# Kernel optimization log

Hardware: AMD Instinct MI355X
Metric: run time of the kernel (lower is better)

Reference implementation:

```python
import jax, jax.numpy as jnp
import numpy as np

N, D, O, E = 8192, 1024, 1024, 16

def setup_inputs() -> dict:
    key = jax.random.key(0)
    k1, k2, k3, k4 = jax.random.split(key, 4)
    scale = 1.0 / np.sqrt(D)
    x = jax.random.normal(k1, (N, D), dtype=jnp.float32)
    Wg = jax.random.normal(k2, (E, D), dtype=jnp.float32) * scale
    We = jax.random.normal(k3, (E, O, D), dtype=jnp.float32) * scale
    be = jax.random.normal(k4, (E, O), dtype=jnp.float32) * scale
    return {"x": x, "Wg": Wg, "We": We, "be": be}

def reference(x, Wg, We, be):
    # gate: softmax over experts
    gate_logits = jnp.einsum('nd,ed->ne', x, Wg)          # [N, E]
    gate_weights = jax.nn.softmax(gate_logits, axis=1)    # [N, E]
    # top-1 mask via >= max (ties keep all maxima, matching torch code)
    max_w = jnp.max(gate_weights, axis=1, keepdims=True)
    mask = (gate_weights >= max_w).astype(gate_weights.dtype)
    sw = gate_weights * mask                              # selected weights [N, E]
    # weighted sum of all-expert Linear outputs, fused (no [N,E,O] intermediate)
    out = jnp.einsum('nd,eod,ne->no', x, We, sw) + sw @ be  # [N, O]
    return (out, gate_weights)
```

## Files before the change

kernel.cpp:

```cpp
#include <hip/hip_runtime.h>
#include <hip/hip_bf16.h>

#define NROWS 8192
#define DIM   1024
#define OUTD  1024
#define NE    16
#define BM    128
#define BN    128
#define BK    32
#define MAXT  96
#define NKSTEP (DIM / BK)
#define NTILE  (OUTD / BN)

typedef short s16x8 __attribute__((ext_vector_type(8)));
typedef float f32x4 __attribute__((ext_vector_type(4)));

__device__ __forceinline__ unsigned f2bf(float f) {
  __hip_bfloat16 h = __float2bfloat16(f);
  return (unsigned)__builtin_bit_cast(unsigned short, h);
}

__global__ void init_kernel(int* counts) {
  int t = threadIdx.x;
  if (t < 32) counts[t] = 0;
}

__global__ __launch_bounds__(256) void gate_kernel(
    const float* __restrict__ x, const float* __restrict__ Wg,
    float* __restrict__ gate_out, int* __restrict__ eid, float* __restrict__ wsel)
{
  __shared__ __align__(16) float wg_lds[NE * 512];
  int t = threadIdx.x;
  int wid = t >> 6, lane = t & 63;
  int n0 = blockIdx.x * 16 + wid * 4;

  float acc[4][NE];
  #pragma unroll
  for (int r = 0; r < 4; ++r)
    #pragma unroll
    for (int e = 0; e < NE; ++e) acc[r][e] = 0.f;

  const float4* wg4 = (const float4*)Wg;
  float4* wl4 = (float4*)wg_lds;

  for (int half = 0; half < 2; ++half) {
    __syncthreads();
    for (int i = t; i < NE * 128; i += 256) {
      int e = i >> 7, c = i & 127;
      wl4[i] = wg4[e * 256 + half * 128 + c];
    }
    __syncthreads();
    #pragma unroll
    for (int r = 0; r < 4; ++r) {
      const float4* xr = (const float4*)(x + (size_t)(n0 + r) * DIM) + half * 128;
      #pragma unroll
      for (int c = 0; c < 2; ++c) {
        float4 xv = xr[lane + c * 64];
        #pragma unroll
        for (int e = 0; e < NE; ++e) {
          float4 wv = wl4[e * 128 + lane + c * 64];
          acc[r][e] += xv.x * wv.x + xv.y * wv.y + xv.z * wv.z + xv.w * wv.w;
        }
      }
    }
  }

  #pragma unroll
  for (int r = 0; r < 4; ++r) {
    int n = n0 + r;
    float p[NE];
    #pragma unroll
    for (int e = 0; e < NE; ++e) {
      float v = acc[r][e];
      #pragma unroll
      for (int off = 32; off; off >>= 1) v += __shfl_xor(v, off, 64);
      p[e] = v;
    }
    float m = p[0];
    #pragma unroll
    for (int e = 1; e < NE; ++e) m = fmaxf(m, p[e]);
    float s = 0.f;
    #pragma unroll
    for (int e = 0; e < NE; ++e) { p[e] = expf(p[e] - m); s += p[e]; }
    float inv = 1.f / s;
    #pragma unroll
    for (int e = 0; e < NE; ++e) p[e] *= inv;
    if (lane == 0) {
      float4* g4 = (float4*)(gate_out + (size_t)n * NE);
      g4[0] = make_float4(p[0], p[1], p[2], p[3]);
      g4[1] = make_float4(p[4], p[5], p[6], p[7]);
      g4[2] = make_float4(p[8], p[9], p[10], p[11]);
      g4[3] = make_float4(p[12], p[13], p[14], p[15]);
      float best = p[0]; int bi = 0;
      #pragma unroll
      for (int e = 1; e < NE; ++e) { if (p[e] > best) { best = p[e]; bi = e; } }
      eid[n] = bi; wsel[n] = best;
    }
  }
}

__global__ __launch_bounds__(256) void count_kernel(
    const int* __restrict__ eid, int* __restrict__ counts)
{
  __shared__ int h[NE];
  int t = threadIdx.x;
  if (t < NE) h[t] = 0;
  __syncthreads();
  int n = blockIdx.x * 256 + t;
  atomicAdd(&h[eid[n]], 1);
  __syncthreads();
  if (t < NE && h[t]) atomicAdd(&counts[t], h[t]);
}

__global__ void plan_kernel(const int* __restrict__ counts,
                            int* __restrict__ offsets, int4* __restrict__ tiles)
{
  int off = 0, tcount = 0;
  for (int e = 0; e < NE; ++e) {
    offsets[e] = off;
    int c = counts[e];
    for (int m = 0; m < c; m += BM)
      tiles[tcount++] = make_int4(e, off + m, (c - m < BM) ? (c - m) : BM, 0);
    off += c;
  }
  offsets[NE] = off;
  for (; tcount < MAXT; ++tcount) tiles[tcount] = make_int4(-1, 0, 0, 0);
}

__global__ __launch_bounds__(256) void scatter_kernel(
    const int* __restrict__ eid, const int* __restrict__ offsets,
    int* __restrict__ cursors, int* __restrict__ rowids)
{
  __shared__ int h[NE];
  __shared__ int base[NE];
  int t = threadIdx.x;
  if (t < NE) h[t] = 0;
  __syncthreads();
  int n = blockIdx.x * 256 + t;
  int e = eid[n];
  int local = atomicAdd(&h[e], 1);
  __syncthreads();
  if (t < NE) base[t] = h[t] ? atomicAdd(&cursors[t], h[t]) : 0;
  __syncthreads();
  rowids[offsets[e] + base[e] + local] = n;
}

__global__ __launch_bounds__(256) void moe_gemm_kernel(
    const float* __restrict__ x, const float* __restrict__ We,
    const float* __restrict__ be, const int* __restrict__ rowids,
    const float* __restrict__ wsel, const int4* __restrict__ tiles,
    float* __restrict__ out)
{
  __shared__ __align__(16) char lds[4 * 8192];
  __shared__ int   rows_s[BM];
  __shared__ float w_s[BM];

  int4 ti = tiles[blockIdx.x];
  int e = ti.x;
  if (e < 0) return;
  int srow = ti.y, nvalid = ti.z;
  int t = threadIdx.x;
  int lane = t & 63, wid = t >> 6;
  int wm = wid >> 1, wn = wid & 1;
  int ncol0 = blockIdx.y * BN;

  if (t < BM) {
    int valid = t < nvalid;
    int rid = valid ? rowids[srow + t] : 0;
    rows_s[t] = valid ? rid : -1;
    w_s[t] = valid ? wsel[rid] : 0.f;
  }
  __syncthreads();

  int tr = t >> 3;
  int tcf = (t & 7) << 2;
  unsigned cg  = (unsigned)(tcf >> 3);
  unsigned sub = (unsigned)((tcf & 7) << 1);
  int ridreg[4];
  #pragma unroll
  for (int j = 0; j < 4; ++j) {
    int rv = rows_s[tr + j * 32];
    ridreg[j] = rv < 0 ? 0 : rv;
  }
  const float* Wbase = We + (size_t)e * OUTD * DIM + (size_t)ncol0 * DIM;

  auto stage = [&](int b, int k0) {
    char* Ab = lds + b * 8192;
    char* Bb = lds + 16384 + b * 8192;
    #pragma unroll
    for (int j = 0; j < 4; ++j) {
      unsigned row = (unsigned)(tr + j * 32);
      unsigned a0 = ((row * 64u + cg * 16u) ^ ((row & 7u) << 4)) + sub;
      float4 v = *(const float4*)(x + (size_t)ridreg[j] * DIM + k0 + tcf);
      unsigned p0 = f2bf(v.x) | (f2bf(v.y) << 16);
      unsigned p1 = f2bf(v.z) | (f2bf(v.w) << 16);
      *(uint2*)(Ab + a0) = make_uint2(p0, p1);
      float4 u = *(const float4*)(Wbase + (size_t)row * DIM + k0 + tcf);
      unsigned q0 = f2bf(u.x) | (f2bf(u.y) << 16);
      unsigned q1 = f2bf(u.z) | (f2bf(u.w) << 16);
      *(uint2*)(Bb + a0) = make_uint2(q0, q1);
    }
  };

  f32x4 zero = {0.f, 0.f, 0.f, 0.f};
  f32x4 acc[4][4];
  #pragma unroll
  for (int i = 0; i < 4; ++i)
    #pragma unroll
    for (int j = 0; j < 4; ++j) acc[i][j] = zero;

  stage(0, 0);

  unsigned rcg  = (unsigned)(lane >> 4);
  unsigned rl15 = (unsigned)(lane & 15);

  for (int ks = 0; ks < NKSTEP; ++ks) {
    __syncthreads();
    if (ks + 1 < NKSTEP) stage((ks + 1) & 1, (ks + 1) * BK);
    char* Ab = lds + (ks & 1) * 8192;
    char* Bb = lds + 16384 + (ks & 1) * 8192;
    s16x8 af[4], bfr[4];
    #pragma unroll
    for (int f = 0; f < 4; ++f) {
      unsigned rA = (unsigned)(wm * 64 + f * 16) + rl15;
      unsigned aA = (rA * 64u + rcg * 16u) ^ ((rA & 7u) << 4);
      af[f] = *(const s16x8*)(Ab + aA);
      unsigned rB = (unsigned)(wn * 64 + f * 16) + rl15;
      unsigned aB = (rB * 64u + rcg * 16u) ^ ((rB & 7u) << 4);
      bfr[f] = *(const s16x8*)(Bb + aB);
    }
    #pragma unroll
    for (int fm = 0; fm < 4; ++fm)
      #pragma unroll
      for (int fn = 0; fn < 4; ++fn)
        acc[fm][fn] = __builtin_amdgcn_mfma_f32_16x16x32_bf16(af[fm], bfr[fn], acc[fm][fn], 0, 0, 0);
  }

  int rgrp = lane >> 4;
  #pragma unroll
  for (int fn = 0; fn < 4; ++fn) {
    int col = ncol0 + wn * 64 + fn * 16 + (lane & 15);
    float bev = be[e * OUTD + col];
    #pragma unroll
    for (int fm = 0; fm < 4; ++fm) {
      #pragma unroll
      for (int j = 0; j < 4; ++j) {
        int rl = wm * 64 + fm * 16 + rgrp * 4 + j;
        int orow = rows_s[rl];
        if (orow >= 0) {
          float w = w_s[rl];
          out[(size_t)orow * OUTD + col] = w * (acc[fm][fn][j] + bev);
        }
      }
    }
  }
}

extern "C" void kernel_launch(void* const* d_in, const int* in_sizes, int n_in,
                              void* d_out, int out_size, void* d_ws, size_t ws_size,
                              hipStream_t stream) {
  const float* x  = (const float*)d_in[0];
  const float* Wg = (const float*)d_in[1];
  const float* We = (const float*)d_in[2];
  const float* be = (const float*)d_in[3];
  float* out = (float*)d_out;
  float* gate_out = out + (size_t)NROWS * OUTD;

  char* ws = (char*)d_ws;
  int*  counts  = (int*)ws;
  int*  cursors = counts + 16;
  int*  offsets = counts + 32;
  int4* tiles   = (int4*)(ws + 256);
  int*  eidp    = (int*)(ws + 4096);
  float* wselp  = (float*)(ws + 4096 + 4 * NROWS);
  int*  rowids  = (int*)(ws + 4096 + 8 * NROWS);

  hipLaunchKernelGGL(init_kernel, dim3(1), dim3(64), 0, stream, counts);
  hipLaunchKernelGGL(gate_kernel, dim3(NROWS / 16), dim3(256), 0, stream,
                     x, Wg, gate_out, eidp, wselp);
  hipLaunchKernelGGL(count_kernel, dim3(NROWS / 256), dim3(256), 0, stream, eidp, counts);
  hipLaunchKernelGGL(plan_kernel, dim3(1), dim3(1), 0, stream, counts, offsets, tiles);
  hipLaunchKernelGGL(scatter_kernel, dim3(NROWS / 256), dim3(256), 0, stream,
                     eidp, offsets, cursors, rowids);
  hipLaunchKernelGGL(moe_gemm_kernel, dim3(MAXT, NTILE), dim3(256), 0, stream,
                     x, We, be, rowids, wselp, tiles, out);
}
```

Baseline: 216.2 us.

## Pre-convert x and We to bf16, use direct global-to-LDS loads, fuse counting into gate

```diff
diff --git a/kernel.cpp b/kernel.cpp
--- a/kernel.cpp
+++ b/kernel.cpp
@@ -20,18 +20,44 @@
   return (unsigned)__builtin_bit_cast(unsigned short, h);
 }
 
+__device__ __forceinline__ void gload_lds16(const void* g, void* l) {
+  __builtin_amdgcn_global_load_lds(
+      (const __attribute__((address_space(1))) void*)g,
+      (__attribute__((address_space(3))) void*)l, 16, 0, 0);
+}
+
 __global__ void init_kernel(int* counts) {
   int t = threadIdx.x;
   if (t < 32) counts[t] = 0;
 }
 
+__global__ __launch_bounds__(256) void convert_we_kernel(
+    const float* __restrict__ W, ushort* __restrict__ o) {
+  size_t i = ((size_t)blockIdx.x * 256 + threadIdx.x) * 8;
+  float4 a = *(const float4*)(W + i);
+  float4 b = *(const float4*)(W + i + 4);
+  unsigned w0 = f2bf(a.x) | (f2bf(a.y) << 16);
+  unsigned w1 = f2bf(a.z) | (f2bf(a.w) << 16);
+  unsigned w2 = f2bf(b.x) | (f2bf(b.y) << 16);
+  unsigned w3 = f2bf(b.z) | (f2bf(b.w) << 16);
+  *(uint4*)(o + i) = make_uint4(w0, w1, w2, w3);
+}
+
 __global__ __launch_bounds__(256) void gate_kernel(
     const float* __restrict__ x, const float* __restrict__ Wg,
-    float* __restrict__ gate_out, int* __restrict__ eid, float* __restrict__ wsel)
+    float* __restrict__ gate_out, int* __restrict__ eid,
+    float* __restrict__ wsel, ushort* __restrict__ xb,
+    int* __restrict__ counts)
 {
-  __shared__ __align__(16) float wg_lds[NE * 512];
-  int t = threadIdx.x;
-  int wid = t >> 6, lane = t & 63;
+  __shared__ __align__(16) float4 wg4[NE * 256];
+  __shared__ int hist[NE];
+  int t = threadIdx.x, wid = t >> 6, lane = t & 63;
+  if (t < NE) hist[t] = 0;
+  const float4* wgg = (const float4*)Wg;
+  #pragma unroll
+  for (int i = 0; i < 16; ++i) wg4[t + i * 256] = wgg[t + i * 256];
+  __syncthreads();
+
   int n0 = blockIdx.x * 16 + wid * 4;
 
   float acc[4][NE];
@@ -40,91 +66,111 @@
     #pragma unroll
     for (int e = 0; e < NE; ++e) acc[r][e] = 0.f;
 
-  const float4* wg4 = (const float4*)Wg;
-  float4* wl4 = (float4*)wg_lds;
-
-  for (int half = 0; half < 2; ++half) {
-    __syncthreads();
-    for (int i = t; i < NE * 128; i += 256) {
-      int e = i >> 7, c = i & 127;
-      wl4[i] = wg4[e * 256 + half * 128 + c];
-    }
-    __syncthreads();
+  #pragma unroll
+  for (int j = 0; j < 4; ++j) {
+    float4 xv[4];
     #pragma unroll
     for (int r = 0; r < 4; ++r) {
-      const float4* xr = (const float4*)(x + (size_t)(n0 + r) * DIM) + half * 128;
+      xv[r] = *(const float4*)(x + (size_t)(n0 + r) * DIM + j * 256 + 4 * lane);
+      unsigned lo = f2bf(xv[r].x) | (f2bf(xv[r].y) << 16);
+      unsigned hi = f2bf(xv[r].z) | (f2bf(xv[r].w) << 16);
+      *(uint2*)(xb + (size_t)(n0 + r) * DIM + j * 256 + 4 * lane) = make_uint2(lo, hi);
+    }
+    #pragma unroll
+    for (int e = 0; e < NE; ++e) {
+      float4 w = wg4[e * 256 + j * 64 + lane];
       #pragma unroll
-      for (int c = 0; c < 2; ++c) {
-        float4 xv = xr[lane + c * 64];
-        #pragma unroll
-        for (int e = 0; e < NE; ++e) {
-          float4 wv = wl4[e * 128 + lane + c * 64];
-          acc[r][e] += xv.x * wv.x + xv.y * wv.y + xv.z * wv.z + xv.w * wv.w;
-        }
-      }
+      for (int r = 0; r < 4; ++r)
+        acc[r][e] += xv[r].x * w.x + xv[r].y * w.y + xv[r].z * w.z + xv[r].w * w.w;
     }
   }
 
   #pragma unroll
   for (int r = 0; r < 4; ++r) {
     int n = n0 + r;
-    float p[NE];
-    #pragma unroll
-    for (int e = 0; e < NE; ++e) {
-      float v = acc[r][e];
-      #pragma unroll
-      for (int off = 32; off; off >>= 1) v += __shfl_xor(v, off, 64);
-      p[e] = v;
-    }
-    float m = p[0];
-    #pragma unroll
-    for (int e = 1; e < NE; ++e) m = fmaxf(m, p[e]);
-    float s = 0.f;
-    #pragma unroll
-    for (int e = 0; e < NE; ++e) { p[e] = expf(p[e] - m); s += p[e]; }
+    float v[NE];
+    #pragma unroll
+    for (int e = 0; e < NE; ++e) v[e] = acc[r][e];
+    #pragma unroll
+    for (int i = 0; i < 8; ++i) {
+      float send = (lane & 32) ? v[i] : v[i + 8];
+      float recv = __shfl_xor(send, 32, 64);
+      v[i] = ((lane & 32) ? v[i + 8] : v[i]) + recv;
+    }
+    #pragma unroll
+    for (int i = 0; i < 4; ++i) {
+      float send = (lane & 16) ? v[i] : v[i + 4];
+      float recv = __shfl_xor(send, 16, 64);
+      v[i] = ((lane & 16) ? v[i + 4] : v[i]) + recv;
+    }
+    #pragma unroll
+    for (int i = 0; i < 2; ++i) {
+      float send = (lane & 8) ? v[i] : v[i + 2];
+      float recv = __shfl_xor(send, 8, 64);
+      v[i] = ((lane & 8) ? v[i + 2] : v[i]) + recv;
+    }
+    {
+      float send = (lane & 4) ? v[0] : v[1];
+      float recv = __shfl_xor(send, 4, 64);
+      v[0] = ((lane & 4) ? v[1] : v[0]) + recv;
+    }
+    v[0] += __shfl_xor(v[0], 2, 64);
+    v[0] += __shfl_xor(v[0], 1, 64);
+    float lg = v[0];
+    int e = ((lane >> 5) & 1) * 8 + ((lane >> 4) & 1) * 4 +
+            ((lane >> 3) & 1) * 2 + ((lane >> 2) & 1);
+    float m = lg;
+    m = fmaxf(m, __shfl_xor(m, 4, 64));
+    m = fmaxf(m, __shfl_xor(m, 8, 64));
+    m = fmaxf(m, __shfl_xor(m, 16, 64));
+    m = fmaxf(m, __shfl_xor(m, 32, 64));
+    float p = expf(lg - m);
+    float s = p;
+    s += __shfl_xor(s, 4, 64);
+    s += __shfl_xor(s, 8, 64);
+    s += __shfl_xor(s, 16, 64);
+    s += __shfl_xor(s, 32, 64);
     float inv = 1.f / s;
-    #pragma unroll
-    for (int e = 0; e < NE; ++e) p[e] *= inv;
+    if ((lane & 3) == 0) gate_out[(size_t)n * NE + e] = p * inv;
+    unsigned long long msk = __ballot(lg == m);
     if (lane == 0) {
-      float4* g4 = (float4*)(gate_out + (size_t)n * NE);
-      g4[0] = make_float4(p[0], p[1], p[2], p[3]);
-      g4[1] = make_float4(p[4], p[5], p[6], p[7]);
-      g4[2] = make_float4(p[8], p[9], p[10], p[11]);
-      g4[3] = make_float4(p[12], p[13], p[14], p[15]);
-      float best = p[0]; int bi = 0;
-      #pragma unroll
-      for (int e = 1; e < NE; ++e) { if (p[e] > best) { best = p[e]; bi = e; } }
-      eid[n] = bi; wsel[n] = best;
-    }
-  }
-}
-
-__global__ __launch_bounds__(256) void count_kernel(
-    const int* __restrict__ eid, int* __restrict__ counts)
-{
-  __shared__ int h[NE];
-  int t = threadIdx.x;
-  if (t < NE) h[t] = 0;
-  __syncthreads();
-  int n = blockIdx.x * 256 + t;
-  atomicAdd(&h[eid[n]], 1);
-  __syncthreads();
-  if (t < NE && h[t]) atomicAdd(&counts[t], h[t]);
+      int fl = __builtin_ctzll(msk);
+      int ebest = ((fl >> 5) & 1) * 8 + ((fl >> 4) & 1) * 4 +
+                  ((fl >> 3) & 1) * 2 + ((fl >> 2) & 1);
+      eid[n] = ebest;
+      wsel[n] = inv;
+      atomicAdd(&hist[ebest], 1);
+    }
+  }
+  __syncthreads();
+  if (t < NE && hist[t]) atomicAdd(&counts[t], hist[t]);
 }
 
 __global__ void plan_kernel(const int* __restrict__ counts,
                             int* __restrict__ offsets, int4* __restrict__ tiles)
 {
-  int off = 0, tcount = 0;
-  for (int e = 0; e < NE; ++e) {
-    offsets[e] = off;
-    int c = counts[e];
-    for (int m = 0; m < c; m += BM)
-      tiles[tcount++] = make_int4(e, off + m, (c - m < BM) ? (c - m) : BM, 0);
-    off += c;
-  }
-  offsets[NE] = off;
-  for (; tcount < MAXT; ++tcount) tiles[tcount] = make_int4(-1, 0, 0, 0);
+  int lane = threadIdx.x;
+  int c = (lane < NE) ? counts[lane] : 0;
+  int nt = (c + BM - 1) >> 7;
+  int po = c, pt = nt;
+  #pragma unroll
+  for (int d = 1; d < 16; d <<= 1) {
+    int oc = __shfl_up(po, d, 64);
+    int ot = __shfl_up(pt, d, 64);
+    if (lane >= d) { po += oc; pt += ot; }
+  }
+  int off = po - c;
+  int tbase = pt - nt;
+  if (lane < NE) offsets[lane] = off;
+  if (lane == NE - 1) offsets[NE] = po;
+  int total_t = __shfl(pt, NE - 1, 64);
+  if (lane < NE) {
+    int ti = 0;
+    for (int m = 0; m < c; m += BM, ++ti)
+      tiles[tbase + ti] = make_int4(lane, off + m, (c - m < BM) ? (c - m) : BM, 0);
+  }
+  for (int i = total_t + lane; i < MAXT; i += 64)
+    tiles[i] = make_int4(-1, 0, 0, 0);
 }
 
 __global__ __launch_bounds__(256) void scatter_kernel(
@@ -146,12 +192,12 @@
 }
 
 __global__ __launch_bounds__(256) void moe_gemm_kernel(
-    const float* __restrict__ x, const float* __restrict__ We,
+    const ushort* __restrict__ xb, const ushort* __restrict__ Web,
     const float* __restrict__ be, const int* __restrict__ rowids,
     const float* __restrict__ wsel, const int4* __restrict__ tiles,
     float* __restrict__ out)
 {
-  __shared__ __align__(16) char lds[4 * 8192];
+  __shared__ __align__(16) char lds[32768];
   __shared__ int   rows_s[BM];
   __shared__ float w_s[BM];
 
@@ -159,9 +205,8 @@
   int e = ti.x;
   if (e < 0) return;
   int srow = ti.y, nvalid = ti.z;
-  int t = threadIdx.x;
-  int lane = t & 63, wid = t >> 6;
-  int wm = wid >> 1, wn = wid & 1;
+  int t = threadIdx.x, lane = t & 63;
+  int wid = t >> 6, wm = wid >> 1, wn = wid & 1;
   int ncol0 = blockIdx.y * BN;
 
   if (t < BM) {
@@ -170,37 +215,17 @@
     rows_s[t] = valid ? rid : -1;
     w_s[t] = valid ? wsel[rid] : 0.f;
   }
-  __syncthreads();
-
-  int tr = t >> 3;
-  int tcf = (t & 7) << 2;
-  unsigned cg  = (unsigned)(tcf >> 3);
-  unsigned sub = (unsigned)((tcf & 7) << 1);
-  int ridreg[4];
-  #pragma unroll
-  for (int j = 0; j < 4; ++j) {
-    int rv = rows_s[tr + j * 32];
-    ridreg[j] = rv < 0 ? 0 : rv;
-  }
-  const float* Wbase = We + (size_t)e * OUTD * DIM + (size_t)ncol0 * DIM;
-
-  auto stage = [&](int b, int k0) {
-    char* Ab = lds + b * 8192;
-    char* Bb = lds + 16384 + b * 8192;
-    #pragma unroll
-    for (int j = 0; j < 4; ++j) {
-      unsigned row = (unsigned)(tr + j * 32);
-      unsigned a0 = ((row * 64u + cg * 16u) ^ ((row & 7u) << 4)) + sub;
-      float4 v = *(const float4*)(x + (size_t)ridreg[j] * DIM + k0 + tcf);
-      unsigned p0 = f2bf(v.x) | (f2bf(v.y) << 16);
-      unsigned p1 = f2bf(v.z) | (f2bf(v.w) << 16);
-      *(uint2*)(Ab + a0) = make_uint2(p0, p1);
-      float4 u = *(const float4*)(Wbase + (size_t)row * DIM + k0 + tcf);
-      unsigned q0 = f2bf(u.x) | (f2bf(u.y) << 16);
-      unsigned q1 = f2bf(u.z) | (f2bf(u.w) << 16);
-      *(uint2*)(Bb + a0) = make_uint2(q0, q1);
-    }
-  };
+
+  int r1 = t >> 2, sl = t & 3;
+  int r2 = r1 + 64;
+  int cg = sl ^ ((r1 >> 1) & 3);
+  int rida1 = (r1 < nvalid) ? rowids[srow + r1] : 0;
+  int rida2 = (r2 < nvalid) ? rowids[srow + r2] : 0;
+  const ushort* ap1 = xb + (size_t)rida1 * DIM + cg * 8;
+  const ushort* ap2 = xb + (size_t)rida2 * DIM + cg * 8;
+  const ushort* bb  = Web + (size_t)e * OUTD * DIM + (size_t)ncol0 * DIM + cg * 8;
+  const ushort* bp1 = bb + (size_t)r1 * DIM;
+  const ushort* bp2 = bb + (size_t)r2 * DIM;
 
   f32x4 zero = {0.f, 0.f, 0.f, 0.f};
   f32x4 acc[4][4];
@@ -209,31 +234,35 @@
     #pragma unroll
     for (int j = 0; j < 4; ++j) acc[i][j] = zero;
 
+  auto stage = [&](int b, int koff) {
+    char* A = lds + b * 8192;
+    char* B = lds + 16384 + b * 8192;
+    gload_lds16(ap1 + koff, A + t * 16);
+    gload_lds16(ap2 + koff, A + 4096 + t * 16);
+    gload_lds16(bp1 + koff, B + t * 16);
+    gload_lds16(bp2 + koff, B + 4096 + t * 16);
+  };
   stage(0, 0);
 
-  unsigned rcg  = (unsigned)(lane >> 4);
-  unsigned rl15 = (unsigned)(lane & 15);
-
+  unsigned rl15 = lane & 15, rcg = lane >> 4;
   for (int ks = 0; ks < NKSTEP; ++ks) {
     __syncthreads();
     if (ks + 1 < NKSTEP) stage((ks + 1) & 1, (ks + 1) * BK);
-    char* Ab = lds + (ks & 1) * 8192;
-    char* Bb = lds + 16384 + (ks & 1) * 8192;
-    s16x8 af[4], bfr[4];
+    const char* A = lds + (ks & 1) * 8192;
+    const char* B = lds + 16384 + (ks & 1) * 8192;
+    s16x8 af[4], bf_[4];
     #pragma unroll
     for (int f = 0; f < 4; ++f) {
-      unsigned rA = (unsigned)(wm * 64 + f * 16) + rl15;
-      unsigned aA = (rA * 64u + rcg * 16u) ^ ((rA & 7u) << 4);
-      af[f] = *(const s16x8*)(Ab + aA);
-      unsigned rB = (unsigned)(wn * 64 + f * 16) + rl15;
-      unsigned aB = (rB * 64u + rcg * 16u) ^ ((rB & 7u) << 4);
-      bfr[f] = *(const s16x8*)(Bb + aB);
+      unsigned rA = wm * 64 + f * 16 + rl15;
+      af[f] = *(const s16x8*)(A + rA * 64 + ((rcg ^ ((rA >> 1) & 3)) * 16));
+      unsigned rB = wn * 64 + f * 16 + rl15;
+      bf_[f] = *(const s16x8*)(B + rB * 64 + ((rcg ^ ((rB >> 1) & 3)) * 16));
     }
     #pragma unroll
     for (int fm = 0; fm < 4; ++fm)
       #pragma unroll
       for (int fn = 0; fn < 4; ++fn)
-        acc[fm][fn] = __builtin_amdgcn_mfma_f32_16x16x32_bf16(af[fm], bfr[fn], acc[fm][fn], 0, 0, 0);
+        acc[fm][fn] = __builtin_amdgcn_mfma_f32_16x16x32_bf16(af[fm], bf_[fn], acc[fm][fn], 0, 0, 0);
   }
 
   int rgrp = lane >> 4;
@@ -274,14 +303,16 @@
   int*  eidp    = (int*)(ws + 4096);
   float* wselp  = (float*)(ws + 4096 + 4 * NROWS);
   int*  rowids  = (int*)(ws + 4096 + 8 * NROWS);
+  ushort* xb    = (ushort*)(ws + (1u << 20));
+  ushort* Web   = (ushort*)(ws + (1u << 20) + 16777216u);
 
   hipLaunchKernelGGL(init_kernel, dim3(1), dim3(64), 0, stream, counts);
+  hipLaunchKernelGGL(convert_we_kernel, dim3(8192), dim3(256), 0, stream, We, Web);
   hipLaunchKernelGGL(gate_kernel, dim3(NROWS / 16), dim3(256), 0, stream,
-                     x, Wg, gate_out, eidp, wselp);
-  hipLaunchKernelGGL(count_kernel, dim3(NROWS / 256), dim3(256), 0, stream, eidp, counts);
-  hipLaunchKernelGGL(plan_kernel, dim3(1), dim3(1), 0, stream, counts, offsets, tiles);
+                     x, Wg, gate_out, eidp, wselp, xb, counts);
+  hipLaunchKernelGGL(plan_kernel, dim3(1), dim3(64), 0, stream, counts, offsets, tiles);
   hipLaunchKernelGGL(scatter_kernel, dim3(NROWS / 256), dim3(256), 0, stream,
                      eidp, offsets, cursors, rowids);
   hipLaunchKernelGGL(moe_gemm_kernel, dim3(MAXT, NTILE), dim3(256), 0, stream,
-                     x, We, be, rowids, wselp, tiles, out);
-}
+                     xb, Web, be, rowids, wselp, tiles, out);
+}
```

New measurement: 221.8 us. +2.6%, slower.
